# Optimization experiments

Hardware: AMD Instinct MI355X
Metric: run time of the kernel (lower is better)

Reference implementation:

```python
import jax, jax.numpy as jnp
import numpy as np

N_NODES = 50000
N_EDGES = 800000
N_GRAPHS = 64
IN_C, HID_C, OUT_C, N_CLS = 128, 128, 64, 2


def _linear_params(key, fan_in, fan_out):
    kw, kb = jax.random.split(key)
    s = 1.0 / np.sqrt(fan_in)
    W = jax.random.uniform(kw, (fan_out, fan_in), jnp.float32, -s, s)
    b = jax.random.uniform(kb, (fan_out,), jnp.float32, -s, s)
    return W, b


def setup_inputs() -> dict:
    key = jax.random.key(0)
    ks = jax.random.split(key, 12)
    x = jax.random.normal(ks[0], (N_NODES, IN_C), jnp.float32)
    edge_index = jax.random.randint(ks[1], (2, N_EDGES), 0, N_NODES, jnp.int32)
    batch = jnp.sort(jax.random.randint(ks[2], (N_NODES,), 0, N_GRAPHS, jnp.int32))
    inp = {"x": x, "edge_index": edge_index, "batch": batch}
    # conv1 params (in=128 -> hid=128): key, query, value, skip linears
    for i, nm in enumerate(["k", "q", "v", "s"]):
        W, b = _linear_params(ks[3 + i], IN_C, HID_C)
        inp[f"w1{nm}"], inp[f"b1{nm}"] = W, b
    # conv2 params (hid=128 -> 64)
    for i, nm in enumerate(["k", "q", "v", "s"]):
        W, b = _linear_params(ks[7 + i], HID_C, OUT_C)
        inp[f"w2{nm}"], inp[f"b2{nm}"] = W, b
    wfc, bfc = _linear_params(ks[11], OUT_C, N_CLS)
    inp["wfc"], inp["bfc"] = wfc, bfc
    return inp


def _res_gated_conv(x, src, dst, Wk, bk, Wq, bq, Wv, bv, Ws, bs):
    # PyG ResGatedGraphConv: eta_ij = sigmoid(k_i + q_j), out_i = skip(x_i) + sum_j eta_ij * v_j
    k = x @ Wk.T + bk  # [N, C_out] (target transform)
    q = x @ Wq.T + bq  # [N, C_out] (source transform)
    v = x @ Wv.T + bv  # [N, C_out]
    eta = jax.nn.sigmoid(k[dst] + q[src])          # [E, C_out]
    msg = eta * v[src]                              # [E, C_out]
    agg = jax.ops.segment_sum(msg, dst, num_segments=x.shape[0])
    return agg + (x @ Ws.T + bs)


def reference(x, edge_index, batch,
              w1k, b1k, w1q, b1q, w1v, b1v, w1s, b1s,
              w2k, b2k, w2q, b2q, w2v, b2v, w2s, b2s,
              wfc, bfc):
    src, dst = edge_index[0], edge_index[1]
    h = jax.nn.relu(_res_gated_conv(x, src, dst, w1k, b1k, w1q, b1q, w1v, b1v, w1s, b1s))
    h = jax.nn.relu(_res_gated_conv(h, src, dst, w2k, b2k, w2q, b2q, w2v, b2v, w2s, b2s))
    # global_mean_pool over graphs
    sums = jax.ops.segment_sum(h, batch, num_segments=N_GRAPHS)            # [G, 64]
    cnts = jax.ops.segment_sum(jnp.ones((h.shape[0],), h.dtype), batch, num_segments=N_GRAPHS)
    pooled = sums / jnp.maximum(cnts, 1.0)[:, None]
    # dropout is identity in eval mode
    return pooled @ wfc.T + bfc  # [G, num_classes]
```

## Files before the change

### kernel.cpp

```cpp
#include <hip/hip_runtime.h>
#include <hip/hip_bf16.h>
#include <math.h>

#define N_NODES 50000
#define N_EDGES 800000
#define N_GRAPHS 64
#define SCAN_BLOCKS 196

typedef __attribute__((ext_vector_type(8))) short short8v;
typedef __attribute__((ext_vector_type(4))) float float4v;

static constexpr size_t OFF_K1   = 0;
static constexpr size_t OFF_S1   = 12800000;
static constexpr size_t OFF_QV1  = 25600000;
static constexpr size_t OFF_H1B  = 51200000;
static constexpr size_t OFF_XB   = 64000000;
static constexpr size_t OFF_K2   = 0;
static constexpr size_t OFF_S2   = 6400000;
static constexpr size_t OFF_QV2  = 12800000;
static constexpr size_t OFF_H2   = 25600000;
static constexpr size_t OFF_ESRC = 76800000;
static constexpr size_t OFF_OFFS = 80000000;
static constexpr size_t OFF_CURS = 80200064;
static constexpr size_t OFF_BSUM = 80400064;
static constexpr size_t OFF_BBAS = 80400848;
static constexpr size_t OFF_BP1  = 80401664;
static constexpr size_t OFF_BC1  = 80532736;
static constexpr size_t OFF_BP2  = 80534784;
static constexpr size_t OFF_BC2  = 80600320;
static constexpr size_t OFF_SG   = 80601344;
static constexpr size_t OFF_EG   = 80601600;
static constexpr size_t OFF_PL   = 80601856;

#define NLOG2E 1.44269504f

__device__ inline unsigned short f2bf(float f) {
    __hip_bfloat16 h = __float2bfloat16(f);
    union { __hip_bfloat16 h; unsigned short u; } cv;
    cv.h = h;
    return cv.u;
}
__device__ inline float fast_exp2(float x) { float r; asm("v_exp_f32 %0, %1" : "=v"(r) : "v"(x)); return r; }
__device__ inline float fast_rcp (float x) { float r; asm("v_rcp_f32 %0, %1" : "=v"(r) : "v"(x)); return r; }
__device__ inline float u2f(unsigned int u) { union { unsigned int i; float f; } w; w.i = u; return w.f; }

__device__ inline void gacc4(uint4 qv, float k0, float k1, float k2, float k3, float* a) {
    float q0 = u2f(qv.x << 16), v0 = u2f(qv.x & 0xffff0000u);
    float q1 = u2f(qv.y << 16), v1 = u2f(qv.y & 0xffff0000u);
    float q2 = u2f(qv.z << 16), v2 = u2f(qv.z & 0xffff0000u);
    float q3 = u2f(qv.w << 16), v3 = u2f(qv.w & 0xffff0000u);
    a[0] += v0 * fast_rcp(1.f + fast_exp2(k0 + q0));
    a[1] += v1 * fast_rcp(1.f + fast_exp2(k1 + q1));
    a[2] += v2 * fast_rcp(1.f + fast_exp2(k2 + q2));
    a[3] += v3 * fast_rcp(1.f + fast_exp2(k3 + q3));
}

__global__ void cast_kernel(const float* __restrict__ x, unsigned short* __restrict__ xb) {
    int id = blockIdx.x * 256 + threadIdx.x;
    float4 v0 = *(const float4*)&x[(size_t)id * 8];
    float4 v1 = *(const float4*)&x[(size_t)id * 8 + 4];
    short8v o;
    o[0] = (short)f2bf(v0.x); o[1] = (short)f2bf(v0.y);
    o[2] = (short)f2bf(v0.z); o[3] = (short)f2bf(v0.w);
    o[4] = (short)f2bf(v1.x); o[5] = (short)f2bf(v1.y);
    o[6] = (short)f2bf(v1.z); o[7] = (short)f2bf(v1.w);
    *(short8v*)(xb + (size_t)id * 8) = o;
}

__global__ void prep1_kernel(const float* __restrict__ wk, const float* __restrict__ bk,
                             const float* __restrict__ wq, const float* __restrict__ bq,
                             const float* __restrict__ wv, const float* __restrict__ bv,
                             const float* __restrict__ ws, const float* __restrict__ bs,
                             unsigned short* __restrict__ Bp, float* __restrict__ bcat) {
    int id = blockIdx.x * 256 + threadIdx.x;
    if (id < 8192) {
        int l = id & 63, ks = (id >> 6) & 3, ct = id >> 8;
        int c = ct * 16 + (l & 15);
        int g = c >> 7, n = c & 127;
        const float* W = (g == 0) ? wk : (g == 1) ? wq : (g == 2) ? wv : ws;
        int kb = ks * 32 + ((l >> 4) << 3);
        short8v o;
#pragma unroll
        for (int j = 0; j < 8; ++j) o[j] = (short)f2bf(W[n * 128 + kb + j]);
        *(short8v*)(Bp + (size_t)id * 8) = o;
    }
    if (id < 512) {
        int g = id >> 7, n = id & 127;
        const float* B = (g == 0) ? bk : (g == 1) ? bq : (g == 2) ? bv : bs;
        bcat[id] = B[n];
    }
}

__global__ void prep2_kernel(const float* __restrict__ wk, const float* __restrict__ bk,
                             const float* __restrict__ wq, const float* __restrict__ bq,
                             const float* __restrict__ wv, const float* __restrict__ bv,
                             const float* __restrict__ ws, const float* __restrict__ bs,
                             unsigned short* __restrict__ Bp, float* __restrict__ bcat) {
    int id = blockIdx.x * 256 + threadIdx.x;
    if (id < 4096) {
        int l = id & 63, ks = (id >> 6) & 3, ct = id >> 8;
        int c = ct * 16 + (l & 15);
        int g = c >> 6, n = c & 63;
        const float* W = (g == 0) ? wk : (g == 1) ? wq : (g == 2) ? wv : ws;
        int kb = ks * 32 + ((l >> 4) << 3);
        short8v o;
#pragma unroll
        for (int j = 0; j < 8; ++j) o[j] = (short)f2bf(W[n * 128 + kb + j]);
        *(short8v*)(Bp + (size_t)id * 8) = o;
    }
    if (id < 256) {
        int g = id >> 6, n = id & 63;
        const float* B = (g == 0) ? bk : (g == 1) ? bq : (g == 2) ? bv : bs;
        bcat[id] = B[n];
    }
}

__global__ void hist_kernel(const int* __restrict__ dst, int* __restrict__ hist) {
    int e = blockIdx.x * 256 + threadIdx.x;
    if (e < N_EDGES) atomicAdd(&hist[dst[e]], 1);
}

__global__ void bsum_kernel(const int* __restrict__ hist, int* __restrict__ bsum) {
    int t = threadIdx.x;
    int idx = blockIdx.x * 256 + t;
    __shared__ int sh[256];
    sh[t] = (idx < N_NODES) ? hist[idx] : 0;
    __syncthreads();
    for (int d = 128; d > 0; d >>= 1) {
        if (t < d) sh[t] += sh[t + d];
        __syncthreads();
    }
    if (t == 0) bsum[blockIdx.x] = sh[0];
}

__global__ void bscan_kernel(const int* __restrict__ bsum, int* __restrict__ bbase) {
    int t = threadIdx.x;
    __shared__ int sh[256];
    sh[t] = (t < SCAN_BLOCKS) ? bsum[t] : 0;
    __syncthreads();
    for (int d = 1; d < 256; d <<= 1) {
        int v = (t >= d) ? sh[t - d] : 0;
        __syncthreads();
        sh[t] += v;
        __syncthreads();
    }
    if (t < SCAN_BLOCKS) bbase[t] = (t == 0) ? 0 : sh[t - 1];
}

__global__ void offs_kernel(const int* __restrict__ hist, const int* __restrict__ bbase,
                            int* __restrict__ offs, int* __restrict__ cursor) {
    int t = threadIdx.x;
    int idx = blockIdx.x * 256 + t;
    int v = (idx < N_NODES) ? hist[idx] : 0;
    __shared__ int sh[256];
    sh[t] = v;
    __syncthreads();
    for (int d = 1; d < 256; d <<= 1) {
        int u = (t >= d) ? sh[t - d] : 0;
        __syncthreads();
        sh[t] += u;
        __syncthreads();
    }
    if (idx < N_NODES) {
        int o = bbase[blockIdx.x] + sh[t] - v;
        offs[idx] = o;
        cursor[idx] = o;
    }
    if (idx == 0) offs[N_NODES] = N_EDGES;
}

__global__ void fill_kernel(const int* __restrict__ src, const int* __restrict__ dst,
                            int* __restrict__ cursor, int* __restrict__ esrc) {
    int e = blockIdx.x * 256 + threadIdx.x;
    if (e < N_EDGES) {
        int d = dst[e];
        int pos = atomicAdd(&cursor[d], 1);
        esrc[pos] = src[e];
    }
}

__global__ __launch_bounds__(256) void gemm1_kernel(const unsigned short* __restrict__ Ab,
                                                    const unsigned short* __restrict__ Bp,
                                                    const float* __restrict__ bias,
                                                    unsigned short* __restrict__ Kout,
                                                    unsigned short* __restrict__ Sout,
                                                    unsigned short* __restrict__ QVout,
                                                    int M) {
    __shared__ __align__(16) unsigned char As[32768];
    const int tid = threadIdx.x;
    const int w = tid >> 6, l = tid & 63;
    const int lx = l & 15, lg = l >> 4;
    const int row0 = blockIdx.x * 128;
    const bool isKS = (blockIdx.y == 0);

#pragma unroll
    for (int i = 0; i < 8; ++i) {
        int id = i * 256 + tid;
        int r = id >> 4, c = id & 15;
        int gr = row0 + r;
        short8v v;
#pragma unroll
        for (int j = 0; j < 8; ++j) v[j] = 0;
        if (gr < M) v = *(const short8v*)(Ab + (size_t)gr * 128 + c * 8);
        *(short8v*)(As + r * 256 + ((c ^ (r & 7)) << 4)) = v;
    }
    __syncthreads();

    float4v acc[2][16];
#pragma unroll
    for (int m = 0; m < 2; ++m)
#pragma unroll
        for (int n = 0; n < 16; ++n)
#pragma unroll
            for (int q = 0; q < 4; ++q) acc[m][n][q] = 0.f;

    const int ctA = isKS ? 0 : 8;
    const int ctB = isKS ? 24 : 16;
#pragma unroll
    for (int ks = 0; ks < 4; ++ks) {
        short8v a[2];
#pragma unroll
        for (int m = 0; m < 2; ++m) {
            int rl = 32 * w + 16 * m + lx;
            int cc = ks * 4 + lg;
            a[m] = *(const short8v*)(As + rl * 256 + ((cc ^ (rl & 7)) << 4));
        }
#pragma unroll
        for (int n = 0; n < 16; ++n) {
            int ct = (n < 8) ? (ctA + n) : (ctB + n - 8);
            short8v b = *(const short8v*)(Bp + (size_t)((ct * 4 + ks) * 64 + l) * 8);
            acc[0][n] = __builtin_amdgcn_mfma_f32_16x16x32_bf16(a[0], b, acc[0][n], 0, 0, 0);
            acc[1][n] = __builtin_amdgcn_mfma_f32_16x16x32_bf16(a[1], b, acc[1][n], 0, 0, 0);
        }
    }

    const int colA0 = isKS ? 0 : 128;
    const int colB0 = isKS ? 384 : 256;
    float bbA[8], bbB[8];
#pragma unroll
    for (int n = 0; n < 8; ++n) {
        bbA[n] = bias[colA0 + 16 * n + lx];
        bbB[n] = bias[colB0 + 16 * n + lx];
    }

    const int rl0 = 32 * w + 4 * lg;
    if (isKS) {
        for (int plane = 0; plane < 2; ++plane) {
            __syncthreads();
#pragma unroll
            for (int m = 0; m < 2; ++m)
#pragma unroll
                for (int reg = 0; reg < 4; ++reg) {
                    int r = rl0 + 16 * m + reg;
#pragma unroll
                    for (int n = 0; n < 8; ++n) {
                        float val = acc[m][plane * 8 + n][reg] + (plane ? bbB[n] : bbA[n]);
                        if (plane == 0) val = -NLOG2E * val;
                        int c = 16 * n + lx;
                        int off = r * 256 + (((c >> 3) ^ (r & 7)) << 4) + ((c & 7) << 1);
                        *(unsigned short*)(As + off) = f2bf(val);
                    }
                }
            __syncthreads();
            unsigned short* Out = plane ? Sout : Kout;
#pragma unroll
            for (int i = 0; i < 8; ++i) {
                int id = i * 256 + tid;
                int row = id >> 4, k = id & 15;
                int gr = row0 + row;
                if (gr < M) {
                    short8v v = *(const short8v*)(As + row * 256 + ((k ^ (row & 7)) << 4));
                    *(short8v*)(Out + (size_t)gr * 128 + k * 8) = v;
                }
            }
        }
    } else {
        for (int h = 0; h < 2; ++h) {
            __syncthreads();
#pragma unroll
            for (int m = 0; m < 2; ++m)
#pragma unroll
                for (int reg = 0; reg < 4; ++reg) {
                    int r = rl0 + 16 * m + reg;
                    if ((r >> 6) == h) {
                        int rr = r & 63;
#pragma unroll
                        for (int n = 0; n < 8; ++n) {
                            float qval = -NLOG2E * (acc[m][n][reg] + bbA[n]);
                            float vval = acc[m][8 + n][reg] + bbB[n];
                            int c = 16 * n + lx;
                            int off = rr * 512 + (((c >> 2) ^ (rr & 7)) << 4) + ((c & 3) << 2);
                            *(unsigned short*)(As + off)     = f2bf(qval);
                            *(unsigned short*)(As + off + 2) = f2bf(vval);
                        }
                    }
                }
            __syncthreads();
#pragma unroll
            for (int i = 0; i < 8; ++i) {
                int id = i * 256 + tid;
                int row = id >> 5, k = id & 31;
                int gr = row0 + h * 64 + row;
                if (gr < M) {
                    short8v v = *(const short8v*)(As + row * 512 + ((k ^ (row & 7)) << 4));
                    *(short8v*)(QVout + (size_t)gr * 256 + k * 8) = v;
                }
            }
        }
    }
}

__global__ __launch_bounds__(256) void gemm2_kernel(const unsigned short* __restrict__ Ab,
                                                    const unsigned short* __restrict__ Bp,
                                                    const float* __restrict__ bias,
                                                    unsigned short* __restrict__ Kout,
                                                    unsigned short* __restrict__ Sout,
                                                    unsigned short* __restrict__ QVout,
                                                    int M) {
    __shared__ __align__(16) unsigned char As[32768];
    const int tid = threadIdx.x;
    const int w = tid >> 6, l = tid & 63;
    const int lx = l & 15, lg = l >> 4;
    const int row0 = blockIdx.x * 128;

#pragma unroll
    for (int i = 0; i < 8; ++i) {
        int id = i * 256 + tid;
        int r = id >> 4, c = id & 15;
        int gr = row0 + r;
        short8v v;
#pragma unroll
        for (int j = 0; j < 8; ++j) v[j] = 0;
        if (gr < M) v = *(const short8v*)(Ab + (size_t)gr * 128 + c * 8);
        *(short8v*)(As + r * 256 + ((c ^ (r & 7)) << 4)) = v;
    }
    __syncthreads();

    float4v acc[2][16];
#pragma unroll
    for (int m = 0; m < 2; ++m)
#pragma unroll
        for (int n = 0; n < 16; ++n)
#pragma unroll
            for (int q = 0; q < 4; ++q) acc[m][n][q] = 0.f;

#pragma unroll
    for (int ks = 0; ks < 4; ++ks) {
        short8v a[2];
#pragma unroll
        for (int m = 0; m < 2; ++m) {
            int rl = 32 * w + 16 * m + lx;
            int cc = ks * 4 + lg;
            a[m] = *(const short8v*)(As + rl * 256 + ((cc ^ (rl & 7)) << 4));
        }
#pragma unroll
        for (int n = 0; n < 16; ++n) {
            short8v b = *(const short8v*)(Bp + (size_t)((n * 4 + ks) * 64 + l) * 8);
            acc[0][n] = __builtin_amdgcn_mfma_f32_16x16x32_bf16(a[0], b, acc[0][n], 0, 0, 0);
            acc[1][n] = __builtin_amdgcn_mfma_f32_16x16x32_bf16(a[1], b, acc[1][n], 0, 0, 0);
        }
    }

    float bbk[4], bbq[4], bbv[4], bbs[4];
#pragma unroll
    for (int n = 0; n < 4; ++n) {
        bbk[n] = bias[16 * n + lx];
        bbq[n] = bias[64 + 16 * n + lx];
        bbv[n] = bias[128 + 16 * n + lx];
        bbs[n] = bias[192 + 16 * n + lx];
    }

    const int rl0 = 32 * w + 4 * lg;
    __syncthreads();
#pragma unroll
    for (int m = 0; m < 2; ++m)
#pragma unroll
        for (int reg = 0; reg < 4; ++reg) {
            int r = rl0 + 16 * m + reg;
#pragma unroll
            for (int n = 0; n < 4; ++n) {
                int c = 16 * n + lx;
                int off = r * 128 + (((c >> 3) ^ (r & 7)) << 4) + ((c & 7) << 1);
                float kv = -NLOG2E * (acc[m][n][reg] + bbk[n]);
                float sv = acc[m][12 + n][reg] + bbs[n];
                *(unsigned short*)(As + off)         = f2bf(kv);
                *(unsigned short*)(As + 16384 + off) = f2bf(sv);
            }
        }
    __syncthreads();
#pragma unroll
    for (int i = 0; i < 8; ++i) {
        int id = i * 256 + tid;
        int half = id >> 10;
        int id2 = id & 1023;
        int row = id2 >> 3, k = id2 & 7;
        int gr = row0 + row;
        if (gr < M) {
            short8v v = *(const short8v*)(As + half * 16384 + row * 128 + ((k ^ (row & 7)) << 4));
            unsigned short* Out = half ? Sout : Kout;
            *(short8v*)(Out + (size_t)gr * 64 + k * 8) = v;
        }
    }
    __syncthreads();
#pragma unroll
    for (int m = 0; m < 2; ++m)
#pragma unroll
        for (int reg = 0; reg < 4; ++reg) {
            int r = rl0 + 16 * m + reg;
#pragma unroll
            for (int n = 0; n < 4; ++n) {
                int c = 16 * n + lx;
                int off = r * 256 + (((c >> 2) ^ (r & 7)) << 4) + ((c & 3) << 2);
                float qv_ = -NLOG2E * (acc[m][4 + n][reg] + bbq[n]);
                float vv  = acc[m][8 + n][reg] + bbv[n];
                *(unsigned short*)(As + off)     = f2bf(qv_);
                *(unsigned short*)(As + off + 2) = f2bf(vv);
            }
        }
    __syncthreads();
#pragma unroll
    for (int i = 0; i < 8; ++i) {
        int id = i * 256 + tid;
        int row = id >> 4, k = id & 15;
        int gr = row0 + row;
        if (gr < M) {
            short8v v = *(const short8v*)(As + row * 256 + ((k ^ (row & 7)) << 4));
            *(short8v*)(QVout + (size_t)gr * 128 + k * 8) = v;
        }
    }
}

__global__ __launch_bounds__(256) void edge1_kernel(const unsigned short* __restrict__ K1b,
                                                    const unsigned short* __restrict__ S1b,
                                                    const unsigned int* __restrict__ QV,
                                                    const int* __restrict__ offs,
                                                    const int* __restrict__ esrc,
                                                    unsigned short* __restrict__ H1B) {
    int node = __builtin_amdgcn_readfirstlane(blockIdx.x * 4 + (threadIdx.x >> 6));
    int lane = threadIdx.x & 63;
    int half = lane >> 5, cl = lane & 31;
    uint2 kk = *(const uint2*)(K1b + (size_t)node * 128 + cl * 4);
    uint2 ss = *(const uint2*)(S1b + (size_t)node * 128 + cl * 4);
    float k0 = u2f(kk.x << 16), k1 = u2f(kk.x & 0xffff0000u);
    float k2 = u2f(kk.y << 16), k3 = u2f(kk.y & 0xffff0000u);
    float a0[4] = {0.f, 0.f, 0.f, 0.f};
    float a1[4] = {0.f, 0.f, 0.f, 0.f};
    int e0 = offs[node], e1 = offs[node + 1];
    int j = e0;
    for (; j + 8 <= e1; j += 8) {
        int s0 = esrc[j + 0 + half];
        int s1 = esrc[j + 2 + half];
        int s2 = esrc[j + 4 + half];
        int s3 = esrc[j + 6 + half];
        uint4 g0 = *(const uint4*)(QV + (size_t)s0 * 128 + cl * 4);
        uint4 g1 = *(const uint4*)(QV + (size_t)s1 * 128 + cl * 4);
        uint4 g2 = *(const uint4*)(QV + (size_t)s2 * 128 + cl * 4);
        uint4 g3 = *(const uint4*)(QV + (size_t)s3 * 128 + cl * 4);
        gacc4(g0, k0, k1, k2, k3, a0);
        gacc4(g1, k0, k1, k2, k3, a1);
        gacc4(g2, k0, k1, k2, k3, a0);
        gacc4(g3, k0, k1, k2, k3, a1);
    }
    for (; j < e1; j += 2) {
        int jj = j + half;
        if (jj < e1) {
            int s = esrc[jj];
            uint4 g = *(const uint4*)(QV + (size_t)s * 128 + cl * 4);
            gacc4(g, k0, k1, k2, k3, a0);
        }
    }
    float t0 = a0[0] + a1[0], t1 = a0[1] + a1[1];
    float t2 = a0[2] + a1[2], t3 = a0[3] + a1[3];
    t0 += __shfl_xor(t0, 32);
    t1 += __shfl_xor(t1, 32);
    t2 += __shfl_xor(t2, 32);
    t3 += __shfl_xor(t3, 32);
    if (half == 0) {
        float s0 = u2f(ss.x << 16), s1 = u2f(ss.x & 0xffff0000u);
        float s2 = u2f(ss.y << 16), s3 = u2f(ss.y & 0xffff0000u);
        float r0 = s0 + t0, r1 = s1 + t1, r2 = s2 + t2, r3 = s3 + t3;
        ushort4 o;
        o.x = f2bf(r0 > 0.f ? r0 : 0.f);
        o.y = f2bf(r1 > 0.f ? r1 : 0.f);
        o.z = f2bf(r2 > 0.f ? r2 : 0.f);
        o.w = f2bf(r3 > 0.f ? r3 : 0.f);
        *(ushort4*)(H1B + (size_t)node * 128 + cl * 4) = o;
    }
}

__global__ __launch_bounds__(256) void edge2_kernel(const unsigned short* __restrict__ K2b,
                                                    const unsigned short* __restrict__ S2b,
                                                    const unsigned int* __restrict__ QV,
                                                    const int* __restrict__ offs,
                                                    const int* __restrict__ esrc,
                                                    float* __restrict__ H2) {
    int node = __builtin_amdgcn_readfirstlane(blockIdx.x * 4 + (threadIdx.x >> 6));
    int lane = threadIdx.x & 63;
    int quart = lane >> 4, cl = lane & 15;
    uint2 kk = *(const uint2*)(K2b + (size_t)node * 64 + cl * 4);
    uint2 ss = *(const uint2*)(S2b + (size_t)node * 64 + cl * 4);
    float k0 = u2f(kk.x << 16), k1 = u2f(kk.x & 0xffff0000u);
    float k2 = u2f(kk.y << 16), k3 = u2f(kk.y & 0xffff0000u);
    float a0[4] = {0.f, 0.f, 0.f, 0.f};
    float a1[4] = {0.f, 0.f, 0.f, 0.f};
    int e0 = offs[node], e1 = offs[node + 1];
    int j = e0;
    for (; j + 8 <= e1; j += 8) {
        int s0 = esrc[j + quart];
        int s1 = esrc[j + 4 + quart];
        uint4 g0 = *(const uint4*)(QV + (size_t)s0 * 64 + cl * 4);
        uint4 g1 = *(const uint4*)(QV + (size_t)s1 * 64 + cl * 4);
        gacc4(g0, k0, k1, k2, k3, a0);
        gacc4(g1, k0, k1, k2, k3, a1);
    }
    for (; j < e1; j += 4) {
        int jj = j + quart;
        if (jj < e1) {
            int s = esrc[jj];
            uint4 g = *(const uint4*)(QV + (size_t)s * 64 + cl * 4);
            gacc4(g, k0, k1, k2, k3, a0);
        }
    }
    float t0 = a0[0] + a1[0], t1 = a0[1] + a1[1];
    float t2 = a0[2] + a1[2], t3 = a0[3] + a1[3];
    t0 += __shfl_xor(t0, 16); t0 += __shfl_xor(t0, 32);
    t1 += __shfl_xor(t1, 16); t1 += __shfl_xor(t1, 32);
    t2 += __shfl_xor(t2, 16); t2 += __shfl_xor(t2, 32);
    t3 += __shfl_xor(t3, 16); t3 += __shfl_xor(t3, 32);
    if (quart == 0) {
        float s0 = u2f(ss.x << 16), s1 = u2f(ss.x & 0xffff0000u);
        float s2 = u2f(ss.y << 16), s3 = u2f(ss.y & 0xffff0000u);
        float4 o;
        o.x = fmaxf(s0 + t0, 0.f);
        o.y = fmaxf(s1 + t1, 0.f);
        o.z = fmaxf(s2 + t2, 0.f);
        o.w = fmaxf(s3 + t3, 0.f);
        *(float4*)(H2 + (size_t)node * 64 + cl * 4) = o;
    }
}

__global__ void bounds_kernel(const int* __restrict__ batch, int* __restrict__ sg,
                              int* __restrict__ eg) {
    int n = blockIdx.x * 256 + threadIdx.x;
    if (n >= N_NODES) return;
    int b = batch[n];
    if (n == 0) {
        sg[b] = 0;
    } else {
        int p = batch[n - 1];
        if (p != b) { sg[b] = n; eg[p] = n - 1; }
    }
    if (n == N_NODES - 1) eg[b] = N_NODES - 1;
}

__global__ void pool_kernel(const float* __restrict__ H2, const int* __restrict__ sg,
                            const int* __restrict__ eg, float* __restrict__ pooled) {
    int g = blockIdx.x;
    int s = sg[g], e = eg[g];
    int ch = threadIdx.x & 63, sub = threadIdx.x >> 6;
    float acc = 0.f;
    for (int n = s + sub; n <= e; n += 4) acc += H2[(size_t)n * 64 + ch];
    __shared__ float red[4][64];
    red[sub][ch] = acc;
    __syncthreads();
    if (sub == 0) {
        float v = red[0][ch] + red[1][ch] + red[2][ch] + red[3][ch];
        int cnt = e - s + 1;
        if (cnt < 1) cnt = 1;
        pooled[g * 64 + ch] = v / (float)cnt;
    }
}

__global__ void fc_kernel(const float* __restrict__ pooled, const float* __restrict__ wfc,
                          const float* __restrict__ bfc, float* __restrict__ out) {
    int t = threadIdx.x;
    int g = t >> 1, c = t & 1;
    float s = bfc[c];
#pragma unroll
    for (int i = 0; i < 64; ++i) s += pooled[g * 64 + i] * wfc[c * 64 + i];
    out[g * 2 + c] = s;
}

extern "C" void kernel_launch(void* const* d_in, const int* in_sizes, int n_in,
                              void* d_out, int out_size, void* d_ws, size_t ws_size,
                              hipStream_t stream) {
    (void)in_sizes; (void)n_in; (void)out_size; (void)ws_size;
    const float* x    = (const float*)d_in[0];
    const int*   ei   = (const int*)d_in[1];
    const int*   batch= (const int*)d_in[2];
    const float* w1k = (const float*)d_in[3];  const float* b1k = (const float*)d_in[4];
    const float* w1q = (const float*)d_in[5];  const float* b1q = (const float*)d_in[6];
    const float* w1v = (const float*)d_in[7];  const float* b1v = (const float*)d_in[8];
    const float* w1s = (const float*)d_in[9];  const float* b1s = (const float*)d_in[10];
    const float* w2k = (const float*)d_in[11]; const float* b2k = (const float*)d_in[12];
    const float* w2q = (const float*)d_in[13]; const float* b2q = (const float*)d_in[14];
    const float* w2v = (const float*)d_in[15]; const float* b2v = (const float*)d_in[16];
    const float* w2s = (const float*)d_in[17]; const float* b2s = (const float*)d_in[18];
    const float* wfc = (const float*)d_in[19]; const float* bfc = (const float*)d_in[20];
    float* out = (float*)d_out;

    char* ws = (char*)d_ws;
    unsigned short* K1  = (unsigned short*)(ws + OFF_K1);
    unsigned short* S1  = (unsigned short*)(ws + OFF_S1);
    unsigned short* QV1 = (unsigned short*)(ws + OFF_QV1);
    unsigned short* H1B = (unsigned short*)(ws + OFF_H1B);
    unsigned short* XB  = (unsigned short*)(ws + OFF_XB);
    unsigned short* K2  = (unsigned short*)(ws + OFF_K2);
    unsigned short* S2  = (unsigned short*)(ws + OFF_S2);
    unsigned short* QV2 = (unsigned short*)(ws + OFF_QV2);
    float* H2   = (float*)(ws + OFF_H2);
    int*   esrc = (int*)(ws + OFF_ESRC);
    int*   offs = (int*)(ws + OFF_OFFS);
    int*   curs = (int*)(ws + OFF_CURS);
    int*   bsum = (int*)(ws + OFF_BSUM);
    int*   bbas = (int*)(ws + OFF_BBAS);
    unsigned short* BP1 = (unsigned short*)(ws + OFF_BP1);
    float* bc1  = (float*)(ws + OFF_BC1);
    unsigned short* BP2 = (unsigned short*)(ws + OFF_BP2);
    float* bc2  = (float*)(ws + OFF_BC2);
    int*   sg   = (int*)(ws + OFF_SG);
    int*   eg   = (int*)(ws + OFF_EG);
    float* pl   = (float*)(ws + OFF_PL);

    const int* src = ei;
    const int* dst = ei + N_EDGES;

    prep1_kernel<<<32, 256, 0, stream>>>(w1k, b1k, w1q, b1q, w1v, b1v, w1s, b1s, BP1, bc1);
    prep2_kernel<<<16, 256, 0, stream>>>(w2k, b2k, w2q, b2q, w2v, b2v, w2s, b2s, BP2, bc2);
    cast_kernel<<<3125, 256, 0, stream>>>(x, XB);

    hipMemsetAsync(curs, 0, N_NODES * sizeof(int), stream);
    hist_kernel<<<(N_EDGES + 255) / 256, 256, 0, stream>>>(dst, curs);
    bsum_kernel<<<SCAN_BLOCKS, 256, 0, stream>>>(curs, bsum);
    bscan_kernel<<<1, 256, 0, stream>>>(bsum, bbas);
    offs_kernel<<<SCAN_BLOCKS, 256, 0, stream>>>(curs, bbas, offs, curs);
    fill_kernel<<<(N_EDGES + 255) / 256, 256, 0, stream>>>(src, dst, curs, esrc);

    gemm1_kernel<<<dim3(391, 2), 256, 0, stream>>>(XB, BP1, bc1, K1, S1, QV1, N_NODES);
    edge1_kernel<<<12500, 256, 0, stream>>>(K1, S1, (const unsigned int*)QV1, offs, esrc, H1B);

    gemm2_kernel<<<391, 256, 0, stream>>>(H1B, BP2, bc2, K2, S2, QV2, N_NODES);
    edge2_kernel<<<12500, 256, 0, stream>>>(K2, S2, (const unsigned int*)QV2, offs, esrc, H2);

    hipMemsetAsync(sg, 0x7f, N_GRAPHS * sizeof(int), stream);
    hipMemsetAsync(eg, 0x80, N_GRAPHS * sizeof(int), stream);
    bounds_kernel<<<(N_NODES + 255) / 256, 256, 0, stream>>>(batch, sg, eg);
    pool_kernel<<<N_GRAPHS, 256, 0, stream>>>(H2, sg, eg, pl);
    fc_kernel<<<1, 128, 0, stream>>>(pl, wfc, bfc, out);
}
```

Baseline: 340.6 us.

## Split node feature tensors into channel-group planes for cache-local edge gathers

Result: slower. 495.3 us (+45.4%).

```diff
diff --git a/kernel.cpp b/kernel.cpp
--- a/kernel.cpp
+++ b/kernel.cpp
@@ -244,6 +244,8 @@
     }
 
     const int rl0 = 32 * w + 4 * lg;
+    unsigned short* lds16 = (unsigned short*)As;
+
     if (isKS) {
         for (int plane = 0; plane < 2; ++plane) {
             __syncthreads();
@@ -256,9 +258,8 @@
                     for (int n = 0; n < 8; ++n) {
                         float val = acc[m][plane * 8 + n][reg] + (plane ? bbB[n] : bbA[n]);
                         if (plane == 0) val = -NLOG2E * val;
-                        int c = 16 * n + lx;
-                        int off = r * 256 + (((c >> 3) ^ (r & 7)) << 4) + ((c & 7) << 1);
-                        *(unsigned short*)(As + off) = f2bf(val);
+                        int eff = (lx >> 3) ^ ((r >> 2) & 1);
+                        lds16[(n * 4096 + r * 32 + (eff << 4) + (lx & 7) * 2) >> 1] = f2bf(val);
                     }
                 }
             __syncthreads();
@@ -266,11 +267,13 @@
 #pragma unroll
             for (int i = 0; i < 8; ++i) {
                 int id = i * 256 + tid;
-                int row = id >> 4, k = id & 15;
-                int gr = row0 + row;
+                int g = id >> 8, rem = id & 255;
+                int r = rem >> 1, half = rem & 1;
+                int eff = half ^ ((r >> 2) & 1);
+                int gr = row0 + r;
                 if (gr < M) {
-                    short8v v = *(const short8v*)(As + row * 256 + ((k ^ (row & 7)) << 4));
-                    *(short8v*)(Out + (size_t)gr * 128 + k * 8) = v;
+                    short8v v = *(const short8v*)(As + g * 4096 + r * 32 + (eff << 4));
+                    *(short8v*)(Out + (size_t)g * 800000 + gr * 16 + half * 8) = v;
                 }
             }
         }
@@ -288,10 +291,10 @@
                         for (int n = 0; n < 8; ++n) {
                             float qval = -NLOG2E * (acc[m][n][reg] + bbA[n]);
                             float vval = acc[m][8 + n][reg] + bbB[n];
-                            int c = 16 * n + lx;
-                            int off = rr * 512 + (((c >> 2) ^ (rr & 7)) << 4) + ((c & 3) << 2);
-                            *(unsigned short*)(As + off)     = f2bf(qval);
-                            *(unsigned short*)(As + off + 2) = f2bf(vval);
+                            int eff = (lx >> 2) ^ ((rr >> 2) & 3);
+                            int off = n * 4096 + rr * 64 + (eff << 4) + (lx & 3) * 4;
+                            lds16[off >> 1]       = f2bf(qval);
+                            lds16[(off >> 1) + 1] = f2bf(vval);
                         }
                     }
                 }
@@ -299,18 +302,20 @@
 #pragma unroll
             for (int i = 0; i < 8; ++i) {
                 int id = i * 256 + tid;
-                int row = id >> 5, k = id & 31;
-                int gr = row0 + h * 64 + row;
+                int g = id >> 8, rem = id & 255;
+                int rr = rem >> 2, ch = rem & 3;
+                int eff = ch ^ ((rr >> 2) & 3);
+                int gr = row0 + h * 64 + rr;
                 if (gr < M) {
-                    short8v v = *(const short8v*)(As + row * 512 + ((k ^ (row & 7)) << 4));
-                    *(short8v*)(QVout + (size_t)gr * 256 + k * 8) = v;
+                    short8v v = *(const short8v*)(As + g * 4096 + rr * 64 + (eff << 4));
+                    *(short8v*)(QVout + (size_t)g * 1600000 + gr * 32 + ch * 8) = v;
                 }
             }
         }
     }
 }
 
-__global__ __launch_bounds__(256) void gemm2_kernel(const unsigned short* __restrict__ Ab,
+__global__ __launch_bounds__(256) void gemm2_kernel(const unsigned short* __restrict__ H1g,
                                                     const unsigned short* __restrict__ Bp,
                                                     const float* __restrict__ bias,
                                                     unsigned short* __restrict__ Kout,
@@ -322,17 +327,20 @@
     const int w = tid >> 6, l = tid & 63;
     const int lx = l & 15, lg = l >> 4;
     const int row0 = blockIdx.x * 128;
+    unsigned short* lds16 = (unsigned short*)As;
 
 #pragma unroll
     for (int i = 0; i < 8; ++i) {
         int id = i * 256 + tid;
-        int r = id >> 4, c = id & 15;
+        int g = id >> 8, rem = id & 255;
+        int r = rem >> 1, half = rem & 1;
         int gr = row0 + r;
         short8v v;
 #pragma unroll
         for (int j = 0; j < 8; ++j) v[j] = 0;
-        if (gr < M) v = *(const short8v*)(Ab + (size_t)gr * 128 + c * 8);
-        *(short8v*)(As + r * 256 + ((c ^ (r & 7)) << 4)) = v;
+        if (gr < M) v = *(const short8v*)(H1g + (size_t)g * 800000 + gr * 16 + half * 8);
+        int cc = 2 * g + half;
+        *(short8v*)(As + r * 256 + ((cc ^ (r & 7)) << 4)) = v;
     }
     __syncthreads();
 
@@ -380,25 +388,23 @@
 #pragma unroll
             for (int n = 0; n < 4; ++n) {
                 int c = 16 * n + lx;
-                int off = r * 128 + (((c >> 3) ^ (r & 7)) << 4) + ((c & 7) << 1);
-                float kv = -NLOG2E * (acc[m][n][reg] + bbk[n]);
-                float sv = acc[m][12 + n][reg] + bbs[n];
-                *(unsigned short*)(As + off)         = f2bf(kv);
-                *(unsigned short*)(As + 16384 + off) = f2bf(sv);
+                int g = c >> 3, cc = c & 7;
+                int off = g * 2048 + r * 16 + cc * 2;
+                lds16[off >> 1]           = f2bf(-NLOG2E * (acc[m][n][reg] + bbk[n]));
+                lds16[(16384 + off) >> 1] = f2bf(acc[m][12 + n][reg] + bbs[n]);
             }
         }
     __syncthreads();
 #pragma unroll
     for (int i = 0; i < 8; ++i) {
         int id = i * 256 + tid;
-        int half = id >> 10;
-        int id2 = id & 1023;
-        int row = id2 >> 3, k = id2 & 7;
-        int gr = row0 + row;
+        int half = id >> 10, id2 = id & 1023;
+        int g = id2 >> 7, r = id2 & 127;
+        int gr = row0 + r;
         if (gr < M) {
-            short8v v = *(const short8v*)(As + half * 16384 + row * 128 + ((k ^ (row & 7)) << 4));
+            short8v v = *(const short8v*)(As + half * 16384 + g * 2048 + r * 16);
             unsigned short* Out = half ? Sout : Kout;
-            *(short8v*)(Out + (size_t)gr * 64 + k * 8) = v;
+            *(short8v*)(Out + (size_t)g * 400000 + gr * 8) = v;
         }
     }
     __syncthreads();
@@ -410,124 +416,109 @@
 #pragma unroll
             for (int n = 0; n < 4; ++n) {
                 int c = 16 * n + lx;
-                int off = r * 256 + (((c >> 2) ^ (r & 7)) << 4) + ((c & 3) << 2);
-                float qv_ = -NLOG2E * (acc[m][4 + n][reg] + bbq[n]);
-                float vv  = acc[m][8 + n][reg] + bbv[n];
-                *(unsigned short*)(As + off)     = f2bf(qv_);
-                *(unsigned short*)(As + off + 2) = f2bf(vv);
+                int g = c >> 3, cc = c & 7;
+                int eff = (cc >> 2) ^ ((r >> 2) & 1);
+                int off = g * 4096 + r * 32 + (eff << 4) + (cc & 3) * 4;
+                lds16[off >> 1]       = f2bf(-NLOG2E * (acc[m][4 + n][reg] + bbq[n]));
+                lds16[(off >> 1) + 1] = f2bf(acc[m][8 + n][reg] + bbv[n]);
             }
         }
     __syncthreads();
 #pragma unroll
     for (int i = 0; i < 8; ++i) {
         int id = i * 256 + tid;
-        int row = id >> 4, k = id & 15;
-        int gr = row0 + row;
+        int g = id >> 8, rem = id & 255;
+        int r = rem >> 1, ch = rem & 1;
+        int eff = ch ^ ((r >> 2) & 1);
+        int gr = row0 + r;
         if (gr < M) {
-            short8v v = *(const short8v*)(As + row * 256 + ((k ^ (row & 7)) << 4));
-            *(short8v*)(QVout + (size_t)gr * 128 + k * 8) = v;
-        }
-    }
-}
-
-__global__ __launch_bounds__(256) void edge1_kernel(const unsigned short* __restrict__ K1b,
-                                                    const unsigned short* __restrict__ S1b,
-                                                    const unsigned int* __restrict__ QV,
+            short8v v = *(const short8v*)(As + g * 4096 + r * 32 + (eff << 4));
+            *(short8v*)(QVout + (size_t)g * 800000 + gr * 16 + ch * 8) = v;
+        }
+    }
+}
+
+__global__ __launch_bounds__(256) void edge1_kernel(const unsigned short* __restrict__ Kg,
+                                                    const unsigned short* __restrict__ Sg,
+                                                    const unsigned int* __restrict__ QVg,
                                                     const int* __restrict__ offs,
                                                     const int* __restrict__ esrc,
-                                                    unsigned short* __restrict__ H1B) {
-    int node = __builtin_amdgcn_readfirstlane(blockIdx.x * 4 + (threadIdx.x >> 6));
+                                                    unsigned short* __restrict__ H1g) {
+    int bid = blockIdx.x;
+    int cg = bid & 7;
+    int node = __builtin_amdgcn_readfirstlane((bid >> 3) * 4 + (threadIdx.x >> 6));
     int lane = threadIdx.x & 63;
-    int half = lane >> 5, cl = lane & 31;
-    uint2 kk = *(const uint2*)(K1b + (size_t)node * 128 + cl * 4);
-    uint2 ss = *(const uint2*)(S1b + (size_t)node * 128 + cl * 4);
+    int le = lane >> 2, lc = lane & 3;
+    uint2 kk = *(const uint2*)(Kg + (size_t)cg * 800000 + node * 16 + lc * 4);
     float k0 = u2f(kk.x << 16), k1 = u2f(kk.x & 0xffff0000u);
     float k2 = u2f(kk.y << 16), k3 = u2f(kk.y & 0xffff0000u);
-    float a0[4] = {0.f, 0.f, 0.f, 0.f};
-    float a1[4] = {0.f, 0.f, 0.f, 0.f};
+    const unsigned int* Q = QVg + (size_t)cg * 800000;
+    float a[4] = {0.f, 0.f, 0.f, 0.f};
     int e0 = offs[node], e1 = offs[node + 1];
-    int j = e0;
-    for (; j + 8 <= e1; j += 8) {
-        int s0 = esrc[j + 0 + half];
-        int s1 = esrc[j + 2 + half];
-        int s2 = esrc[j + 4 + half];
-        int s3 = esrc[j + 6 + half];
-        uint4 g0 = *(const uint4*)(QV + (size_t)s0 * 128 + cl * 4);
-        uint4 g1 = *(const uint4*)(QV + (size_t)s1 * 128 + cl * 4);
-        uint4 g2 = *(const uint4*)(QV + (size_t)s2 * 128 + cl * 4);
-        uint4 g3 = *(const uint4*)(QV + (size_t)s3 * 128 + cl * 4);
-        gacc4(g0, k0, k1, k2, k3, a0);
-        gacc4(g1, k0, k1, k2, k3, a1);
-        gacc4(g2, k0, k1, k2, k3, a0);
-        gacc4(g3, k0, k1, k2, k3, a1);
-    }
-    for (; j < e1; j += 2) {
-        int jj = j + half;
-        if (jj < e1) {
-            int s = esrc[jj];
-            uint4 g = *(const uint4*)(QV + (size_t)s * 128 + cl * 4);
-            gacc4(g, k0, k1, k2, k3, a0);
-        }
-    }
-    float t0 = a0[0] + a1[0], t1 = a0[1] + a1[1];
-    float t2 = a0[2] + a1[2], t3 = a0[3] + a1[3];
-    t0 += __shfl_xor(t0, 32);
-    t1 += __shfl_xor(t1, 32);
-    t2 += __shfl_xor(t2, 32);
-    t3 += __shfl_xor(t3, 32);
-    if (half == 0) {
+    for (int j0 = e0; j0 < e1; j0 += 16) {
+        int j = j0 + le;
+        if (j < e1) {
+            int s = esrc[j];
+            uint4 g = *(const uint4*)(Q + (size_t)s * 16 + lc * 4);
+            gacc4(g, k0, k1, k2, k3, a);
+        }
+    }
+    float t0 = a[0], t1 = a[1], t2 = a[2], t3 = a[3];
+#pragma unroll
+    for (int mask = 4; mask <= 32; mask <<= 1) {
+        t0 += __shfl_xor(t0, mask);
+        t1 += __shfl_xor(t1, mask);
+        t2 += __shfl_xor(t2, mask);
+        t3 += __shfl_xor(t3, mask);
+    }
+    if (le == 0) {
+        uint2 ss = *(const uint2*)(Sg + (size_t)cg * 800000 + node * 16 + lc * 4);
         float s0 = u2f(ss.x << 16), s1 = u2f(ss.x & 0xffff0000u);
         float s2 = u2f(ss.y << 16), s3 = u2f(ss.y & 0xffff0000u);
-        float r0 = s0 + t0, r1 = s1 + t1, r2 = s2 + t2, r3 = s3 + t3;
         ushort4 o;
-        o.x = f2bf(r0 > 0.f ? r0 : 0.f);
-        o.y = f2bf(r1 > 0.f ? r1 : 0.f);
-        o.z = f2bf(r2 > 0.f ? r2 : 0.f);
-        o.w = f2bf(r3 > 0.f ? r3 : 0.f);
-        *(ushort4*)(H1B + (size_t)node * 128 + cl * 4) = o;
-    }
-}
-
-__global__ __launch_bounds__(256) void edge2_kernel(const unsigned short* __restrict__ K2b,
-                                                    const unsigned short* __restrict__ S2b,
-                                                    const unsigned int* __restrict__ QV,
+        o.x = f2bf(fmaxf(s0 + t0, 0.f));
+        o.y = f2bf(fmaxf(s1 + t1, 0.f));
+        o.z = f2bf(fmaxf(s2 + t2, 0.f));
+        o.w = f2bf(fmaxf(s3 + t3, 0.f));
+        *(ushort4*)(H1g + (size_t)cg * 800000 + node * 16 + lc * 4) = o;
+    }
+}
+
+__global__ __launch_bounds__(256) void edge2_kernel(const unsigned short* __restrict__ Kg,
+                                                    const unsigned short* __restrict__ Sg,
+                                                    const unsigned int* __restrict__ QVg,
                                                     const int* __restrict__ offs,
                                                     const int* __restrict__ esrc,
-                                                    float* __restrict__ H2) {
-    int node = __builtin_amdgcn_readfirstlane(blockIdx.x * 4 + (threadIdx.x >> 6));
+                                                    float* __restrict__ H2g) {
+    int bid = blockIdx.x;
+    int cg = bid & 7;
+    int node = __builtin_amdgcn_readfirstlane((bid >> 3) * 4 + (threadIdx.x >> 6));
     int lane = threadIdx.x & 63;
-    int quart = lane >> 4, cl = lane & 15;
-    uint2 kk = *(const uint2*)(K2b + (size_t)node * 64 + cl * 4);
-    uint2 ss = *(const uint2*)(S2b + (size_t)node * 64 + cl * 4);
+    int le = lane >> 1, lc = lane & 1;
+    uint2 kk = *(const uint2*)(Kg + (size_t)cg * 400000 + node * 8 + lc * 4);
     float k0 = u2f(kk.x << 16), k1 = u2f(kk.x & 0xffff0000u);
     float k2 = u2f(kk.y << 16), k3 = u2f(kk.y & 0xffff0000u);
-    float a0[4] = {0.f, 0.f, 0.f, 0.f};
-    float a1[4] = {0.f, 0.f, 0.f, 0.f};
+    const unsigned int* Q = QVg + (size_t)cg * 400000;
+    float a[4] = {0.f, 0.f, 0.f, 0.f};
     int e0 = offs[node], e1 = offs[node + 1];
-    int j = e0;
-    for (; j + 8 <= e1; j += 8) {
-        int s0 = esrc[j + quart];
-        int s1 = esrc[j + 4 + quart];
-        uint4 g0 = *(const uint4*)(QV + (size_t)s0 * 64 + cl * 4);
-        uint4 g1 = *(const uint4*)(QV + (size_t)s1 * 64 + cl * 4);
-        gacc4(g0, k0, k1, k2, k3, a0);
-        gacc4(g1, k0, k1, k2, k3, a1);
-    }
-    for (; j < e1; j += 4) {
-        int jj = j + quart;
-        if (jj < e1) {
-            int s = esrc[jj];
-            uint4 g = *(const uint4*)(QV + (size_t)s * 64 + cl * 4);
-            gacc4(g, k0, k1, k2, k3, a0);
-        }
-    }
-    float t0 = a0[0] + a1[0], t1 = a0[1] + a1[1];
-    float t2 = a0[2] + a1[2], t3 = a0[3] + a1[3];
-    t0 += __shfl_xor(t0, 16); t0 += __shfl_xor(t0, 32);
-    t1 += __shfl_xor(t1, 16); t1 += __shfl_xor(t1, 32);
-    t2 += __shfl_xor(t2, 16); t2 += __shfl_xor(t2, 32);
-    t3 += __shfl_xor(t3, 16); t3 += __shfl_xor(t3, 32);
-    if (quart == 0) {
+    for (int j0 = e0; j0 < e1; j0 += 32) {
+        int j = j0 + le;
+        if (j < e1) {
+            int s = esrc[j];
+            uint4 g = *(const uint4*)(Q + (size_t)s * 8 + lc * 4);
+            gacc4(g, k0, k1, k2, k3, a);
+        }
+    }
+    float t0 = a[0], t1 = a[1], t2 = a[2], t3 = a[3];
+#pragma unroll
+    for (int mask = 2; mask <= 32; mask <<= 1) {
+        t0 += __shfl_xor(t0, mask);
+        t1 += __shfl_xor(t1, mask);
+        t2 += __shfl_xor(t2, mask);
+        t3 += __shfl_xor(t3, mask);
+    }
+    if (le == 0) {
+        uint2 ss = *(const uint2*)(Sg + (size_t)cg * 400000 + node * 8 + lc * 4);
         float s0 = u2f(ss.x << 16), s1 = u2f(ss.x & 0xffff0000u);
         float s2 = u2f(ss.y << 16), s3 = u2f(ss.y & 0xffff0000u);
         float4 o;
@@ -535,7 +526,7 @@
         o.y = fmaxf(s1 + t1, 0.f);
         o.z = fmaxf(s2 + t2, 0.f);
         o.w = fmaxf(s3 + t3, 0.f);
-        *(float4*)(H2 + (size_t)node * 64 + cl * 4) = o;
+        *(float4*)(H2g + (size_t)cg * 400000 + node * 8 + lc * 4) = o;
     }
 }
 
@@ -553,13 +544,15 @@
     if (n == N_NODES - 1) eg[b] = N_NODES - 1;
 }
 
-__global__ void pool_kernel(const float* __restrict__ H2, const int* __restrict__ sg,
+__global__ void pool_kernel(const float* __restrict__ H2g, const int* __restrict__ sg,
                             const int* __restrict__ eg, float* __restrict__ pooled) {
     int g = blockIdx.x;
     int s = sg[g], e = eg[g];
     int ch = threadIdx.x & 63, sub = threadIdx.x >> 6;
+    int grp = ch >> 3, within = ch & 7;
+    const float* base = H2g + (size_t)grp * 400000 + within;
     float acc = 0.f;
-    for (int n = s + sub; n <= e; n += 4) acc += H2[(size_t)n * 64 + ch];
+    for (int n = s + sub; n <= e; n += 4) acc += base[(size_t)n * 8];
     __shared__ float red[4][64];
     red[sub][ch] = acc;
     __syncthreads();
@@ -637,10 +630,10 @@
     fill_kernel<<<(N_EDGES + 255) / 256, 256, 0, stream>>>(src, dst, curs, esrc);
 
     gemm1_kernel<<<dim3(391, 2), 256, 0, stream>>>(XB, BP1, bc1, K1, S1, QV1, N_NODES);
-    edge1_kernel<<<12500, 256, 0, stream>>>(K1, S1, (const unsigned int*)QV1, offs, esrc, H1B);
+    edge1_kernel<<<100000, 256, 0, stream>>>(K1, S1, (const unsigned int*)QV1, offs, esrc, H1B);
 
     gemm2_kernel<<<391, 256, 0, stream>>>(H1B, BP2, bc2, K2, S2, QV2, N_NODES);
-    edge2_kernel<<<12500, 256, 0, stream>>>(K2, S2, (const unsigned int*)QV2, offs, esrc, H2);
+    edge2_kernel<<<100000, 256, 0, stream>>>(K2, S2, (const unsigned int*)QV2, offs, esrc, H2);
 
     hipMemsetAsync(sg, 0x7f, N_GRAPHS * sizeof(int), stream);
     hipMemsetAsync(eg, 0x80, N_GRAPHS * sizeof(int), stream);
```
